# Optimization experiments

Hardware: AMD Instinct MI355X
Metric: run time of the kernel (lower is better)

The kernel has to match this reference:

```python
import jax, jax.numpy as jnp
import numpy as np

B, K, I, H, O = 256, 512, 64, 512, 1


def setup_inputs() -> dict:
    key = jax.random.key(0)
    ks = jax.random.split(key, 4)
    return {
        "input_seq": jax.random.normal(ks[0], (B, K, I), dtype=jnp.float32),
        "kernel": jax.random.normal(ks[1], (I, 4 * H), dtype=jnp.float32) * (2.0 / I) ** 0.5,
        "recurrent_kernel": jax.random.normal(ks[2], (4 * H, H), dtype=jnp.float32) * (2.0 / H) ** 0.5,
        "bias": jnp.zeros((4 * H,), dtype=jnp.float32),
        "Woutput": jax.random.normal(ks[3], (O, H), dtype=jnp.float32) * (2.0 / H) ** 0.5,
        "boutput": jnp.zeros((O,), dtype=jnp.float32),
    }


def reference(input_seq, kernel, recurrent_kernel, bias, Woutput, boutput):
    Bsz, Kt, _ = input_seq.shape
    Hs = recurrent_kernel.shape[1]
    # Precompute input projections for all timesteps: (K, B, 4H)
    x_proj = jnp.einsum("bki,ig->kbg", input_seq, kernel)

    def step(carry, x_t):
        h, c = carry
        # F.linear(h, recurrent_kernel, bias) == h @ recurrent_kernel.T + bias
        gates = x_t + h @ recurrent_kernel.T + bias  # (B, 4H)
        f_g, i_g, c_g, o_g = jnp.split(gates, 4, axis=1)
        f = jax.nn.sigmoid(f_g)
        i = jax.nn.sigmoid(i_g)
        c_prime = jnp.tanh(c_g)
        c_t = f * c + i * c_prime
        o = jax.nn.sigmoid(o_g)
        h_t = o * jnp.tanh(c_t)
        return (h_t, c_t), None

    h0 = jnp.zeros((Bsz, Hs), dtype=input_seq.dtype)
    c0 = jnp.zeros((Bsz, Hs), dtype=input_seq.dtype)
    (h_last, _), _ = jax.lax.scan(step, (h0, c0), x_proj)
    # Output layer applied to last timestep only (only lstm_out of final step is used)
    out = h_last @ Woutput.T + boutput  # (B, O)
    return out.reshape(-1)
```

## Files before the change

kernel.cpp:

```cpp
#include <hip/hip_runtime.h>

#define TSTEPS 512
#define BATCH  256
#define ISZ    64
#define HSZ    512
#define GSZ    2048
#define NKT    18
#define BG     16
#define PAR_STRIDE 131072

typedef __attribute__((ext_vector_type(8))) short short8;
typedef __attribute__((ext_vector_type(4))) float f32x4;
typedef __attribute__((ext_vector_type(4))) unsigned int u32x4;
typedef unsigned long long u64t;

static __device__ __forceinline__ unsigned short f2bf(float f) {
    unsigned int u = __float_as_uint(f);
    return (unsigned short)((u + 0x7fffu + ((u >> 16) & 1u)) >> 16);
}
static __device__ __forceinline__ float sig_(float x) {
    return 1.0f / (1.0f + __expf(-x));
}
static __device__ __forceinline__ float tanh_(float x) {
    float e = __expf(-2.0f * fabsf(x));
    float t = (1.0f - e) / (1.0f + e);
    return copysignf(t, x);
}
static __device__ __forceinline__ u64t ld_tag64(const u64t* p) {
    return __hip_atomic_load(p, __ATOMIC_RELAXED, __HIP_MEMORY_SCOPE_AGENT);
}
static __device__ __forceinline__ void st_tag64(u64t* p, u64t v) {
    __hip_atomic_store(p, v, __ATOMIC_RELAXED, __HIP_MEMORY_SCOPE_AGENT);
}

__global__ void pack_w(const float* __restrict__ R, const float* __restrict__ Kin,
                       unsigned short* __restrict__ wpack)
{
    const int t  = blockIdx.x * 256 + threadIdx.x;
    const int l  = t & 63;
    const int kt = (t >> 6) % NKT;
    const int m  = (t / (64 * NKT)) & 7;
    const int jj = t / (64 * NKT * 8);
    const int r   = 16 * m + (l & 15);
    const int q   = r & 3;
    const int hco = r >> 2;
    const int grow  = q * HSZ + jj * 32 + hco;
    const int kbase = kt * 32 + (l >> 4) * 8;
    unsigned int pk[4];
#pragma unroll
    for (int p = 0; p < 4; ++p) {
        const int k0 = kbase + 2 * p;
        const int k1 = k0 + 1;
        const float f0 = (k0 < HSZ) ? R[(size_t)grow * HSZ + k0]
                                    : Kin[(size_t)(k0 - HSZ) * GSZ + grow];
        const float f1 = (k1 < HSZ) ? R[(size_t)grow * HSZ + k1]
                                    : Kin[(size_t)(k1 - HSZ) * GSZ + grow];
        pk[p] = (unsigned)f2bf(f0) | ((unsigned)f2bf(f1) << 16);
    }
    uint4 v = make_uint4(pk[0], pk[1], pk[2], pk[3]);
    *reinterpret_cast<uint4*>(wpack + (size_t)t * 8) = v;
}

__global__ void zero_tags(u32x4* __restrict__ hb) {
    u32x4 z = {0u, 0u, 0u, 0u};
    hb[blockIdx.x * 256 + threadIdx.x] = z;
}

__global__ __launch_bounds__(512, 1) void lstm_persist(
    const unsigned short* __restrict__ wpack,
    const float* __restrict__ input_seq,
    const float* __restrict__ bias,
    unsigned int* __restrict__ tbuf,
    float* __restrict__ hlast)
{
    __shared__ __align__(16) unsigned short lds_B[16][584];
    __shared__ __align__(16) unsigned short lds_hn[16][68];
    const int tid = threadIdx.x;
    const int bid = blockIdx.x;
    const int gi = (bid & 7) + 8 * (bid >> 6);
    const int jw = (bid >> 3) & 7;

    const int w  = tid >> 6;
    const int l  = tid & 63;
    const int bb = l & 15;
    const int lg = l >> 4;
    const int jj = 2 * jw + (w >> 2);
    const int mw = w & 3;
    const int m0 = 2 * mw, m1 = 2 * mw + 1;

    short8 wA[NKT], wB[NKT];
#pragma unroll
    for (int kt = 0; kt < NKT; ++kt) {
        wA[kt] = *reinterpret_cast<const short8*>(
            wpack + (((size_t)(jj * 8 + m0) * NKT + kt) * 64 + l) * 8);
        wB[kt] = *reinterpret_cast<const short8*>(
            wpack + (((size_t)(jj * 8 + m1) * NKT + kt) * 64 + l) * 8);
    }
#pragma unroll
    for (int kt = 0; kt < NKT; ++kt) {
        asm volatile("" : "+a"(wA[kt]));
        asm volatile("" : "+a"(wB[kt]));
    }
    const int hc0 = 4 * m0 + lg, hc1 = 4 * m1 + lg;
    const int gh0 = jj * 32 + hc0, gh1 = jj * 32 + hc1;
    float bs0[4], bs1[4];
#pragma unroll
    for (int qg = 0; qg < 4; ++qg) {
        bs0[qg] = bias[qg * HSZ + gh0];
        bs1[qg] = bias[qg * HSZ + gh1];
    }

    float c0 = 0.f, c1 = 0.f;

    const int sb = tid & 15, sc = tid >> 4;
    const float* xbase = input_seq + (size_t)(gi * BG + sb) * (TSTEPS * ISZ) + sc * 2;
    float2 xr = *reinterpret_cast<const float2*>(xbase);

    const u64t* const hb0 = reinterpret_cast<const u64t*>(tbuf);
    const u64t* const hb1 = reinterpret_cast<const u64t*>(tbuf + (size_t)PAR_STRIDE);
    const int rr = tid >> 5, cch = tid & 31;
    const size_t csrc = (size_t)(gi * BG + rr) * 256 + cch;
    const int b_ = tid >> 5, pr = tid & 31;
    const size_t pdst = ((size_t)(gi * BG + b_) * HSZ + jw * 64 + pr * 2) >> 1;

    for (int s = 0; s < TSTEPS; ++s) {
        {
            unsigned px = (unsigned)f2bf(xr.x) | ((unsigned)f2bf(xr.y) << 16);
            *reinterpret_cast<unsigned*>(&lds_B[sb][HSZ + sc * 2]) = px;
            if (s + 1 < TSTEPS)
                xr = *reinterpret_cast<const float2*>(xbase + (size_t)(s + 1) * ISZ);
        }
        if (s > 0) {
            const u64t* src = ((s & 1) ? hb1 : hb0) + csrc;
            const u64t want = ((u64t)(unsigned)s << 48) | ((u64t)(unsigned)s << 16);
            u64t v[8];
            bool ok;
            do {
                ok = true;
#pragma unroll
                for (int i = 0; i < 8; ++i)
                    v[i] = ld_tag64(src + (size_t)i * 32);
#pragma unroll
                for (int i = 0; i < 8; ++i)
                    ok = ok && ((v[i] & 0xFFFF0000FFFF0000ull) == want);
            } while (!ok);
#pragma unroll
            for (int i = 0; i < 8; ++i) {
                const unsigned d = (unsigned)(v[i] & 0xFFFFu) |
                                   ((unsigned)(v[i] >> 16) & 0xFFFF0000u);
                *reinterpret_cast<unsigned*>(&lds_B[rr][i * 64 + cch * 2]) = d;
            }
        } else {
#pragma unroll
            for (int i = 0; i < 8; ++i)
                *reinterpret_cast<unsigned*>(&lds_B[rr][i * 64 + cch * 2]) = 0u;
        }
        __syncthreads();

        f32x4 acc0 = {0.f, 0.f, 0.f, 0.f};
        f32x4 acc1 = {0.f, 0.f, 0.f, 0.f};
#pragma unroll
        for (int kt = 0; kt < NKT; ++kt) {
            const short8 bf = *reinterpret_cast<const short8*>(
                &lds_B[bb][kt * 32 + lg * 8]);
            acc0 = __builtin_amdgcn_mfma_f32_16x16x32_bf16(wA[kt], bf, acc0, 0, 0, 0);
            acc1 = __builtin_amdgcn_mfma_f32_16x16x32_bf16(wB[kt], bf, acc1, 0, 0, 0);
        }

        const float fg0 = sig_(acc0[0] + bs0[0]);
        const float ig0 = sig_(acc0[1] + bs0[1]);
        const float cp0 = tanh_(acc0[2] + bs0[2]);
        const float og0 = sig_(acc0[3] + bs0[3]);
        c0 = fg0 * c0 + ig0 * cp0;
        const float h0v = og0 * tanh_(c0);
        const float fg1 = sig_(acc1[0] + bs1[0]);
        const float ig1 = sig_(acc1[1] + bs1[1]);
        const float cp1 = tanh_(acc1[2] + bs1[2]);
        const float og1 = sig_(acc1[3] + bs1[3]);
        c1 = fg1 * c1 + ig1 * cp1;
        const float h1v = og1 * tanh_(c1);

        if (s == TSTEPS - 1) {
            hlast[(size_t)(gi * BG + bb) * HSZ + gh0] = h0v;
            hlast[(size_t)(gi * BG + bb) * HSZ + gh1] = h1v;
            break;
        }
        const int cw = (w >> 2) * 32;
        lds_hn[bb][cw + hc0] = f2bf(h0v);
        lds_hn[bb][cw + hc1] = f2bf(h1v);
        __syncthreads();

        {
            const unsigned h2 = *reinterpret_cast<const unsigned*>(&lds_hn[b_][pr * 2]);
            const unsigned t16 = (unsigned)(s + 1) << 16;
            const unsigned lo = (h2 & 0xFFFFu) | t16;
            const unsigned hi = (h2 >> 16) | t16;
            const u64t tagged = ((u64t)hi << 32) | (u64t)lo;
            u64t* dst = (u64t*)(tbuf + (size_t)((s + 1) & 1) * PAR_STRIDE) + pdst;
            st_tag64(dst, tagged);
        }
    }
}

__global__ void out_kernel(const float* __restrict__ hlast,
                           const float* __restrict__ wout,
                           const float* __restrict__ bout,
                           float* __restrict__ out)
{
    const int b = blockIdx.x;
    const int l = threadIdx.x;
    float p = 0.f;
    for (int k = l; k < HSZ; k += 64)
        p += hlast[(size_t)b * HSZ + k] * wout[k];
    for (int off = 32; off > 0; off >>= 1)
        p += __shfl_down(p, off, 64);
    if (l == 0) out[b] = p + bout[0];
}

extern "C" void kernel_launch(void* const* d_in, const int* in_sizes, int n_in,
                              void* d_out, int out_size, void* d_ws, size_t ws_size,
                              hipStream_t stream) {
    const float* input_seq = (const float*)d_in[0];
    const float* Kin       = (const float*)d_in[1];
    const float* R         = (const float*)d_in[2];
    const float* bias      = (const float*)d_in[3];
    const float* Wout      = (const float*)d_in[4];
    const float* bout      = (const float*)d_in[5];
    float* out = (float*)d_out;

    char* ws = (char*)d_ws;
    unsigned short* wpack = (unsigned short*)(ws);
    unsigned int* tbuf    = (unsigned int*)(ws + 2359296);
    float* hlast          = (float*)(ws + 2359296 + 1048576);

    zero_tags<<<dim3(256), dim3(256), 0, stream>>>((u32x4*)tbuf);
    pack_w<<<dim3(576), dim3(256), 0, stream>>>(R, Kin, wpack);
    lstm_persist<<<dim3(128), dim3(512), 0, stream>>>(
        wpack, input_seq, bias, tbuf, hlast);
    out_kernel<<<dim3(256), dim3(64), 0, stream>>>(hlast, Wout, bout, out);
}
```

Before: 1.347 ms.

## Split persistent LSTM across 256 workgroups of 4 waves each

```diff
diff --git a/kernel.cpp b/kernel.cpp
--- a/kernel.cpp
+++ b/kernel.cpp
@@ -7,7 +7,7 @@
 #define GSZ    2048
 #define NKT    18
 #define BG     16
-#define PAR_STRIDE 131072
+#define PLANE64 65536
 
 typedef __attribute__((ext_vector_type(8))) short short8;
 typedef __attribute__((ext_vector_type(4))) float f32x4;
@@ -66,7 +66,7 @@
     hb[blockIdx.x * 256 + threadIdx.x] = z;
 }
 
-__global__ __launch_bounds__(512, 1) void lstm_persist(
+__global__ __launch_bounds__(256, 1) void lstm_persist(
     const unsigned short* __restrict__ wpack,
     const float* __restrict__ input_seq,
     const float* __restrict__ bias,
@@ -74,19 +74,18 @@
     float* __restrict__ hlast)
 {
     __shared__ __align__(16) unsigned short lds_B[16][584];
-    __shared__ __align__(16) unsigned short lds_hn[16][68];
+    __shared__ __align__(16) unsigned short lds_hn[16][40];
     const int tid = threadIdx.x;
     const int bid = blockIdx.x;
-    const int gi = (bid & 7) + 8 * (bid >> 6);
-    const int jw = (bid >> 3) & 7;
+    const int gi = bid & 15;
+    const int jw = bid >> 4;
+    const int jj = jw;
 
     const int w  = tid >> 6;
     const int l  = tid & 63;
     const int bb = l & 15;
     const int lg = l >> 4;
-    const int jj = 2 * jw + (w >> 2);
-    const int mw = w & 3;
-    const int m0 = 2 * mw, m1 = 2 * mw + 1;
+    const int m0 = 2 * w, m1 = 2 * w + 1;
 
     short8 wA[NKT], wB[NKT];
 #pragma unroll
@@ -113,52 +112,54 @@
     float c0 = 0.f, c1 = 0.f;
 
     const int sb = tid & 15, sc = tid >> 4;
-    const float* xbase = input_seq + (size_t)(gi * BG + sb) * (TSTEPS * ISZ) + sc * 2;
-    float2 xr = *reinterpret_cast<const float2*>(xbase);
+    const float* xbase = input_seq + (size_t)(gi * BG + sb) * (TSTEPS * ISZ) + sc * 4;
+    float4 xr = *reinterpret_cast<const float4*>(xbase);
 
     const u64t* const hb0 = reinterpret_cast<const u64t*>(tbuf);
-    const u64t* const hb1 = reinterpret_cast<const u64t*>(tbuf + (size_t)PAR_STRIDE);
-    const int rr = tid >> 5, cch = tid & 31;
+    const u64t* const hb1 = reinterpret_cast<const u64t*>(tbuf) + PLANE64;
+    const int rr = tid >> 4, cch = tid & 15;
     const size_t csrc = (size_t)(gi * BG + rr) * 256 + cch;
-    const int b_ = tid >> 5, pr = tid & 31;
-    const size_t pdst = ((size_t)(gi * BG + b_) * HSZ + jw * 64 + pr * 2) >> 1;
+    const int b_ = tid >> 4, pr = tid & 15;
+    const size_t pdst = ((size_t)(gi * BG + b_) * HSZ + jw * 32 + pr * 2) >> 1;
 
     for (int s = 0; s < TSTEPS; ++s) {
         {
-            unsigned px = (unsigned)f2bf(xr.x) | ((unsigned)f2bf(xr.y) << 16);
-            *reinterpret_cast<unsigned*>(&lds_B[sb][HSZ + sc * 2]) = px;
+            uint2 px;
+            px.x = (unsigned)f2bf(xr.x) | ((unsigned)f2bf(xr.y) << 16);
+            px.y = (unsigned)f2bf(xr.z) | ((unsigned)f2bf(xr.w) << 16);
+            *reinterpret_cast<uint2*>(&lds_B[sb][HSZ + sc * 4]) = px;
             if (s + 1 < TSTEPS)
-                xr = *reinterpret_cast<const float2*>(xbase + (size_t)(s + 1) * ISZ);
+                xr = *reinterpret_cast<const float4*>(xbase + (size_t)(s + 1) * ISZ);
         }
         if (s > 0) {
             const u64t* src = ((s & 1) ? hb1 : hb0) + csrc;
             const u64t want = ((u64t)(unsigned)s << 48) | ((u64t)(unsigned)s << 16);
-            u64t v[8];
+            u64t v[16];
             bool ok;
             do {
                 ok = true;
 #pragma unroll
-                for (int i = 0; i < 8; ++i)
-                    v[i] = ld_tag64(src + (size_t)i * 32);
-#pragma unroll
-                for (int i = 0; i < 8; ++i)
+                for (int i = 0; i < 16; ++i)
+                    v[i] = ld_tag64(src + (size_t)i * 16);
+#pragma unroll
+                for (int i = 0; i < 16; ++i)
                     ok = ok && ((v[i] & 0xFFFF0000FFFF0000ull) == want);
             } while (!ok);
 #pragma unroll
-            for (int i = 0; i < 8; ++i) {
+            for (int i = 0; i < 16; ++i) {
                 const unsigned d = (unsigned)(v[i] & 0xFFFFu) |
                                    ((unsigned)(v[i] >> 16) & 0xFFFF0000u);
-                *reinterpret_cast<unsigned*>(&lds_B[rr][i * 64 + cch * 2]) = d;
+                *reinterpret_cast<unsigned*>(&lds_B[rr][i * 32 + cch * 2]) = d;
             }
         } else {
 #pragma unroll
-            for (int i = 0; i < 8; ++i)
-                *reinterpret_cast<unsigned*>(&lds_B[rr][i * 64 + cch * 2]) = 0u;
+            for (int i = 0; i < 16; ++i)
+                *reinterpret_cast<unsigned*>(&lds_B[rr][i * 32 + cch * 2]) = 0u;
         }
         __syncthreads();
 
-        f32x4 acc0 = {0.f, 0.f, 0.f, 0.f};
-        f32x4 acc1 = {0.f, 0.f, 0.f, 0.f};
+        f32x4 acc0 = {bs0[0], bs0[1], bs0[2], bs0[3]};
+        f32x4 acc1 = {bs1[0], bs1[1], bs1[2], bs1[3]};
 #pragma unroll
         for (int kt = 0; kt < NKT; ++kt) {
             const short8 bf = *reinterpret_cast<const short8*>(
@@ -167,16 +168,16 @@
             acc1 = __builtin_amdgcn_mfma_f32_16x16x32_bf16(wB[kt], bf, acc1, 0, 0, 0);
         }
 
-        const float fg0 = sig_(acc0[0] + bs0[0]);
-        const float ig0 = sig_(acc0[1] + bs0[1]);
-        const float cp0 = tanh_(acc0[2] + bs0[2]);
-        const float og0 = sig_(acc0[3] + bs0[3]);
+        const float fg0 = sig_(acc0[0]);
+        const float ig0 = sig_(acc0[1]);
+        const float cp0 = tanh_(acc0[2]);
+        const float og0 = sig_(acc0[3]);
         c0 = fg0 * c0 + ig0 * cp0;
         const float h0v = og0 * tanh_(c0);
-        const float fg1 = sig_(acc1[0] + bs1[0]);
-        const float ig1 = sig_(acc1[1] + bs1[1]);
-        const float cp1 = tanh_(acc1[2] + bs1[2]);
-        const float og1 = sig_(acc1[3] + bs1[3]);
+        const float fg1 = sig_(acc1[0]);
+        const float ig1 = sig_(acc1[1]);
+        const float cp1 = tanh_(acc1[2]);
+        const float og1 = sig_(acc1[3]);
         c1 = fg1 * c1 + ig1 * cp1;
         const float h1v = og1 * tanh_(c1);
 
@@ -185,9 +186,8 @@
             hlast[(size_t)(gi * BG + bb) * HSZ + gh1] = h1v;
             break;
         }
-        const int cw = (w >> 2) * 32;
-        lds_hn[bb][cw + hc0] = f2bf(h0v);
-        lds_hn[bb][cw + hc1] = f2bf(h1v);
+        lds_hn[bb][hc0] = f2bf(h0v);
+        lds_hn[bb][hc1] = f2bf(h1v);
         __syncthreads();
 
         {
@@ -196,7 +196,7 @@
             const unsigned lo = (h2 & 0xFFFFu) | t16;
             const unsigned hi = (h2 >> 16) | t16;
             const u64t tagged = ((u64t)hi << 32) | (u64t)lo;
-            u64t* dst = (u64t*)(tbuf + (size_t)((s + 1) & 1) * PAR_STRIDE) + pdst;
+            u64t* dst = (u64t*)(tbuf) + (size_t)((s + 1) & 1) * PLANE64 + pdst;
             st_tag64(dst, tagged);
         }
     }
@@ -235,7 +235,7 @@
 
     zero_tags<<<dim3(256), dim3(256), 0, stream>>>((u32x4*)tbuf);
     pack_w<<<dim3(576), dim3(256), 0, stream>>>(R, Kin, wpack);
-    lstm_persist<<<dim3(128), dim3(512), 0, stream>>>(
+    lstm_persist<<<dim3(256), dim3(256), 0, stream>>>(
         wpack, input_seq, bias, tbuf, hlast);
     out_kernel<<<dim3(256), dim3(64), 0, stream>>>(hlast, Wout, bout, out);
 }
```

Result: faster. 1.129 ms (-16.2%).
